# Optimization experiments

Measured on AMD Instinct MI355X. Metric: run time of the kernel, lower is better.

The kernel has to match this reference:

```python
import jax, jax.numpy as jnp
import numpy as np

B, T, C = 2, 2048, 1024
H, HS = 16, 64
FF = 4 * C
EPS = 1e-5


def _layernorm(x, w):
    mu = jnp.mean(x, axis=-1, keepdims=True)
    var = jnp.var(x, axis=-1, keepdims=True)
    return (x - mu) / jnp.sqrt(var + EPS) * w


def setup_inputs() -> dict:
    key = jax.random.key(0)
    ks = jax.random.split(key, 16)
    s_in = 1.0 / np.sqrt(C)
    s_o = 1.0 / np.sqrt(H * HS)
    s_ff = 1.0 / np.sqrt(FF)
    return {
        "x": jax.random.normal(ks[0], (B, T, C), dtype=jnp.float32),
        "ln1_w": jnp.ones((C,), jnp.float32),
        "Wq": jax.random.uniform(ks[1], (H, C, HS), jnp.float32, -s_in, s_in),
        "bq": jax.random.uniform(ks[2], (H, HS), jnp.float32, -s_in, s_in),
        "Wk": jax.random.uniform(ks[3], (H, C, HS), jnp.float32, -s_in, s_in),
        "bk": jax.random.uniform(ks[4], (H, HS), jnp.float32, -s_in, s_in),
        "Wv": jax.random.uniform(ks[5], (H, C, HS), jnp.float32, -s_in, s_in),
        "bv": jax.random.uniform(ks[6], (H, HS), jnp.float32, -s_in, s_in),
        "Wo": jax.random.uniform(ks[7], (H * HS, C), jnp.float32, -s_o, s_o),
        "bo": jax.random.uniform(ks[8], (C,), jnp.float32, -s_o, s_o),
        "ln2_w": jnp.ones((C,), jnp.float32),
        "W1": jax.random.uniform(ks[9], (C, FF), jnp.float32, -s_in, s_in),
        "b1": jax.random.uniform(ks[10], (FF,), jnp.float32, -s_in, s_in),
        "W2": jax.random.uniform(ks[11], (FF, C), jnp.float32, -s_ff, s_ff),
        "b2": jax.random.uniform(ks[12], (C,), jnp.float32, -s_ff, s_ff),
    }


def reference(x, ln1_w, Wq, bq, Wk, bk, Wv, bv, Wo, bo, ln2_w, W1, b1, W2, b2):
    h = _layernorm(x, ln1_w)                                   # [B,T,C]
    q = jnp.einsum("btc,hcd->bhtd", h, Wq) + bq[:, None, :]    # [B,H,T,HS]
    k = jnp.einsum("btc,hcd->bhtd", h, Wk) + bk[:, None, :]
    v = jnp.einsum("btc,hcd->bhtd", h, Wv) + bv[:, None, :]
    scores = jnp.einsum("bhid,bhjd->bhij", q, k) * (HS ** -0.5)
    causal = jnp.tril(jnp.ones((T, T), bool))                  # tril mask
    scores = jnp.where(causal, scores, -jnp.inf)
    # NOTE: original applies softmax over torch dim=1 of [B,T,T] = query axis i
    w = jax.nn.softmax(scores, axis=2)                         # [B,H,i,j]
    att = jnp.einsum("bhij,bhjd->bhid", w, v)                  # [B,H,T,HS]
    att = att.transpose(0, 2, 1, 3).reshape(B, T, H * HS)      # concat heads
    att = att @ Wo + bo                                        # [B,T,C]
    x1 = x + att
    h2 = _layernorm(x1, ln2_w)
    ff = jax.nn.relu(h2 @ W1 + b1) @ W2 + b2
    return x1 + ff
```

## Files before the change

### kernel.cpp

```cpp
#include <hip/hip_runtime.h>
#include <hip/hip_bf16.h>
#include <stddef.h>
#include <stdint.h>


constexpr int Bn = 2, Tn = 2048, Cn = 1024, Hn = 16, HSn = 64, FFn = 4096;
constexpr int Mn = Bn * Tn;
constexpr float EPSf = 1e-5f;
constexpr float S2 = 0.125f * 1.44269504088896340736f;

using short8 = __attribute__((ext_vector_type(8))) short;
using f32x4  = __attribute__((ext_vector_type(4))) float;
using s16x4  = __attribute__((ext_vector_type(4))) short;

#define DEVINL __device__ __forceinline__

DEVINL unsigned short f2bf(float f) {
  unsigned int u = __float_as_uint(f);
  u += 0x7fffu + ((u >> 16) & 1u);
  return (unsigned short)(u >> 16);
}

#define GLDS16(g, l) __builtin_amdgcn_global_load_lds(                        \
    (const __attribute__((address_space(1))) void*)(g),                       \
    (__attribute__((address_space(3))) void*)(l), 16, 0, 0)

__global__ __launch_bounds__(256)
void transpose_cvt(const float* __restrict__ in, unsigned short* __restrict__ out,
                   int R, int S, long zin, long zout) {
  __shared__ float tile[32][33];
  const int c0 = blockIdx.x * 32;
  const int r0 = blockIdx.y * 32;
  in  += (size_t)blockIdx.z * zin;
  out += (size_t)blockIdx.z * zout;
  const int tid = threadIdx.x;
#pragma unroll
  for (int j = 0; j < 4; ++j) {
    const int f = tid + j * 256;
    tile[f >> 5][f & 31] = in[(size_t)(r0 + (f >> 5)) * S + c0 + (f & 31)];
  }
  __syncthreads();
#pragma unroll
  for (int j = 0; j < 4; ++j) {
    const int f = tid + j * 256;
    const int sr = f >> 5, rc = f & 31;
    out[(size_t)(c0 + sr) * R + r0 + rc] = f2bf(tile[rc][sr]);
  }
}

__global__ __launch_bounds__(256)
void ln_bf16(const float* __restrict__ x, const float* __restrict__ w,
             unsigned short* __restrict__ out) {
  const int row = blockIdx.x, tid = threadIdx.x;
  const float4 v = ((const float4*)(x + (size_t)row * Cn))[tid];
  float s  = v.x + v.y + v.z + v.w;
  float ss = v.x*v.x + v.y*v.y + v.z*v.z + v.w*v.w;
#pragma unroll
  for (int o = 32; o > 0; o >>= 1) { s += __shfl_xor(s, o); ss += __shfl_xor(ss, o); }
  __shared__ float red[8];
  if ((tid & 63) == 0) { red[tid >> 6] = s; red[(tid >> 6) + 4] = ss; }
  __syncthreads();
  s  = red[0] + red[1] + red[2] + red[3];
  ss = red[4] + red[5] + red[6] + red[7];
  const float mu   = s * (1.0f / Cn);
  const float rstd = rsqrtf(ss * (1.0f / Cn) - mu * mu + EPSf);
  const float4 wv = ((const float4*)w)[tid];
  s16x4 o;
  o[0] = (short)f2bf((v.x - mu) * rstd * wv.x);
  o[1] = (short)f2bf((v.y - mu) * rstd * wv.y);
  o[2] = (short)f2bf((v.z - mu) * rstd * wv.z);
  o[3] = (short)f2bf((v.w - mu) * rstd * wv.w);
  ((s16x4*)(out + (size_t)row * Cn))[tid] = o;
}

template <int EPI, int OMODE>
__global__ __launch_bounds__(256)
void gemm_bf16(const unsigned short* __restrict__ A,
               const unsigned short* __restrict__ Bt,
               const float* __restrict__ bias, const float* __restrict__ res,
               void* __restrict__ outp, int M, int N, int K) {
  __shared__ unsigned short As[128][64];
  __shared__ unsigned short Bs[128][64];
  const int tid = threadIdx.x;
  const int w = tid >> 6, l = tid & 63;
  const int wm = w >> 1, wn = w & 1;
  const int m0 = blockIdx.y * 128, n0 = blockIdx.x * 128;
  f32x4 acc[4][4];
#pragma unroll
  for (int i = 0; i < 4; ++i)
#pragma unroll
    for (int j = 0; j < 4; ++j) acc[i][j] = (f32x4){0.f, 0.f, 0.f, 0.f};

  for (int k0 = 0; k0 < K; k0 += 64) {
    __syncthreads();
#pragma unroll
    for (int j = 0; j < 4; ++j) {
      const int chunk = (w * 4 + j) * 64 + l;
      const int row = chunk >> 3, slot = chunk & 7;
      GLDS16(A + (size_t)(m0 + row) * K + k0 + ((slot ^ (row & 7)) << 3),
             &As[0][0] + (size_t)(w * 4 + j) * 512);
    }
#pragma unroll
    for (int j = 0; j < 4; ++j) {
      const int chunk = (w * 4 + j) * 64 + l;
      const int row = chunk >> 3, slot = chunk & 7;
      GLDS16(Bt + (size_t)(n0 + row) * K + k0 + ((slot ^ (row & 7)) << 3),
             &Bs[0][0] + (size_t)(w * 4 + j) * 512);
    }
    __syncthreads();
#pragma unroll
    for (int kk = 0; kk < 2; ++kk) {
      short8 a[4], b[4];
#pragma unroll
      for (int i = 0; i < 4; ++i) {
        const int ar = wm * 64 + i * 16 + (l & 15);
        a[i] = *(const short8*)&As[ar][(((l >> 4) + kk * 4) ^ (ar & 7)) << 3];
        const int br = wn * 64 + i * 16 + (l & 15);
        b[i] = *(const short8*)&Bs[br][(((l >> 4) + kk * 4) ^ (br & 7)) << 3];
      }
#pragma unroll
      for (int mi = 0; mi < 4; ++mi)
#pragma unroll
        for (int ni = 0; ni < 4; ++ni)
          acc[mi][ni] = __builtin_amdgcn_mfma_f32_16x16x32_bf16(
              a[mi], b[ni], acc[mi][ni], 0, 0, 0);
    }
  }
  if (OMODE == 2) {
    unsigned short* vT = (unsigned short*)outp;
#pragma unroll
    for (int mi = 0; mi < 4; ++mi)
#pragma unroll
      for (int ni = 0; ni < 4; ++ni) {
        const int n = n0 + wn * 64 + ni * 16 + (l & 15);
        const int mbase = m0 + wm * 64 + mi * 16 + ((l >> 4) << 2);
        const int bb = mbase >> 11, t = mbase & 2047;
        const float bv = bias[n];
        unsigned short* dst = vT + ((size_t)(bb * 1024 + n)) * Tn + t;
        unsigned int p0 = (unsigned)f2bf(acc[mi][ni][0] + bv) |
                          ((unsigned)f2bf(acc[mi][ni][1] + bv) << 16);
        unsigned int p1 = (unsigned)f2bf(acc[mi][ni][2] + bv) |
                          ((unsigned)f2bf(acc[mi][ni][3] + bv) << 16);
        *(unsigned int*)dst       = p0;
        *(unsigned int*)(dst + 2) = p1;
      }
  } else {
#pragma unroll
    for (int mi = 0; mi < 4; ++mi)
#pragma unroll
      for (int ni = 0; ni < 4; ++ni) {
        const int n = n0 + wn * 64 + ni * 16 + (l & 15);
        const float bv = bias[n];
#pragma unroll
        for (int r = 0; r < 4; ++r) {
          const int m = m0 + wm * 64 + mi * 16 + ((l >> 4) << 2) + r;
          float v = acc[mi][ni][r] + bv;
          if (EPI == 1) v = fmaxf(v, 0.f);
          if (EPI == 2) v += res[(size_t)m * N + n];
          if (OMODE == 1) ((unsigned short*)outp)[(size_t)m * N + n] = f2bf(v);
          else            ((float*)outp)[(size_t)m * N + n] = v;
        }
      }
  }
}

DEVINL void stage64s(unsigned short* lds, const unsigned short* g, int grs,
                     int w, int l) {
#pragma unroll
  for (int j = 0; j < 2; ++j) {
    const int chunk = (w * 2 + j) * 64 + l;
    const int row = chunk >> 3, slot = chunk & 7;
    GLDS16(g + (size_t)row * grs + ((slot ^ (row & 7)) << 3),
           lds + (size_t)(w * 2 + j) * 512);
  }
}

__global__ __launch_bounds__(256)
void colstats_mfma(const unsigned short* __restrict__ qk,
                   float* __restrict__ m2buf, float* __restrict__ rlbuf) {
  __shared__ unsigned short Ks[64][64];
  __shared__ unsigned short Qs[64][64];
  __shared__ float redm[4][4][16], redl[4][4][16];
  const int j0 = blockIdx.x * 64;
  const int bh = blockIdx.y, b = bh >> 4, h = bh & 15;
  const int tid = threadIdx.x, w = tid >> 6, l = tid & 63;
  const unsigned short* kbase = qk + ((size_t)(b * Tn + j0)) * 2048 + 1024 + h * 64;
  const unsigned short* qbase = qk + ((size_t)(b * Tn)) * 2048 + h * 64;
  stage64s(&Ks[0][0], kbase, 2048, w, l);
  float m2[4], ls[4];
#pragma unroll
  for (int ni = 0; ni < 4; ++ni) { m2[ni] = -1e30f; ls[ni] = 0.f; }

  for (int i0 = j0; i0 < Tn; i0 += 64) {
    __syncthreads();
    stage64s(&Qs[0][0], qbase + (size_t)i0 * 2048, 2048, w, l);
    __syncthreads();
    f32x4 s[4];
#pragma unroll
    for (int ni = 0; ni < 4; ++ni) s[ni] = (f32x4){0.f, 0.f, 0.f, 0.f};
#pragma unroll
    for (int kk = 0; kk < 2; ++kk) {
      const int ar = w * 16 + (l & 15);
      const short8 af = *(const short8*)&Qs[ar][(((l >> 4) + kk * 4) ^ (ar & 7)) << 3];
#pragma unroll
      for (int ni = 0; ni < 4; ++ni) {
        const int br = ni * 16 + (l & 15);
        const short8 bfr = *(const short8*)&Ks[br][(((l >> 4) + kk * 4) ^ (br & 7)) << 3];
        s[ni] = __builtin_amdgcn_mfma_f32_16x16x32_bf16(af, bfr, s[ni], 0, 0, 0);
      }
    }
    const bool diag = (i0 == j0);
    const int ib = w * 16 + ((l >> 4) << 2);
#pragma unroll
    for (int ni = 0; ni < 4; ++ni) {
      const int jl = ni * 16 + (l & 15);
      float v0 = s[ni][0] * S2, v1 = s[ni][1] * S2, v2 = s[ni][2] * S2, v3 = s[ni][3] * S2;
      if (!diag) {
        const float tmax = fmaxf(fmaxf(v0, v1), fmaxf(v2, v3));
        const float mn = fmaxf(m2[ni], tmax);
        ls[ni] = ls[ni] * exp2f(m2[ni] - mn) +
                 exp2f(v0 - mn) + exp2f(v1 - mn) + exp2f(v2 - mn) + exp2f(v3 - mn);
        m2[ni] = mn;
      } else {
        const bool g0 = (ib + 0 >= jl), g1 = (ib + 1 >= jl), g2 = (ib + 2 >= jl), g3 = (ib + 3 >= jl);
        const float t0 = g0 ? v0 : -1e30f, t1 = g1 ? v1 : -1e30f;
        const float t2 = g2 ? v2 : -1e30f, t3 = g3 ? v3 : -1e30f;
        const float tmax = fmaxf(fmaxf(t0, t1), fmaxf(t2, t3));
        const float mn = fmaxf(m2[ni], tmax);
        const float e0 = g0 ? exp2f(v0 - mn) : 0.f;
        const float e1 = g1 ? exp2f(v1 - mn) : 0.f;
        const float e2 = g2 ? exp2f(v2 - mn) : 0.f;
        const float e3 = g3 ? exp2f(v3 - mn) : 0.f;
        ls[ni] = ls[ni] * exp2f(m2[ni] - mn) + e0 + e1 + e2 + e3;
        m2[ni] = mn;
      }
    }
  }
#pragma unroll
  for (int ni = 0; ni < 4; ++ni) {
#pragma unroll
    for (int off = 16; off < 64; off <<= 1) {
      const float mo = __shfl_xor(m2[ni], off);
      const float lo = __shfl_xor(ls[ni], off);
      const float mn = fmaxf(m2[ni], mo);
      ls[ni] = ls[ni] * exp2f(m2[ni] - mn) + lo * exp2f(mo - mn);
      m2[ni] = mn;
    }
  }
  if (l < 16) {
#pragma unroll
    for (int ni = 0; ni < 4; ++ni) { redm[w][ni][l] = m2[ni]; redl[w][ni][l] = ls[ni]; }
  }
  __syncthreads();
  if (tid < 64) {
    const int ni = tid >> 4, jl = tid & 15;
    float m = redm[0][ni][jl], sl = redl[0][ni][jl];
#pragma unroll
    for (int wv = 1; wv < 4; ++wv) {
      const float mo = redm[wv][ni][jl], lo = redl[wv][ni][jl];
      const float mn = fmaxf(m, mo);
      sl = sl * exp2f(m - mn) + lo * exp2f(mo - mn);
      m = mn;
    }
    m2buf[(size_t)bh * Tn + j0 + ni * 16 + jl] = m;
    rlbuf[(size_t)bh * Tn + j0 + ni * 16 + jl] = 1.0f / sl;
  }
}

__global__ __launch_bounds__(256)
void pv_mfma(const unsigned short* __restrict__ qk,
             const unsigned short* __restrict__ vT,
             const float* __restrict__ m2buf, const float* __restrict__ rlbuf,
             unsigned short* __restrict__ att) {
  __shared__ unsigned short Qs[64][64];
  __shared__ unsigned short Ks[64][64];
  __shared__ unsigned short Vs[64][64];
  __shared__ unsigned short Ps[64][64];
  __shared__ float m2s[64], rls[64];
  const int i0 = blockIdx.x * 64;
  const int bh = blockIdx.y, b = bh >> 4, h = bh & 15;
  const int tid = threadIdx.x, w = tid >> 6, l = tid & 63;
  const unsigned short* qbase = qk + ((size_t)(b * Tn + i0)) * 2048 + h * 64;
  const unsigned short* kbase = qk + ((size_t)(b * Tn)) * 2048 + 1024 + h * 64;
  const unsigned short* vbase = vT + ((size_t)(b * 1024 + h * 64)) * Tn;
  stage64s(&Qs[0][0], qbase, 2048, w, l);
  f32x4 oacc[4];
#pragma unroll
  for (int ni = 0; ni < 4; ++ni) oacc[ni] = (f32x4){0.f, 0.f, 0.f, 0.f};

  for (int j0 = 0; j0 <= i0; j0 += 64) {
    __syncthreads();
    stage64s(&Ks[0][0], kbase + (size_t)j0 * 2048, 2048, w, l);
#pragma unroll
    for (int j = 0; j < 2; ++j) {
      const int chunk = (w * 2 + j) * 64 + l;
      const int row = chunk >> 3, slot = chunk & 7;
      GLDS16(vbase + (size_t)row * Tn + j0 + ((slot ^ (row & 7)) << 3),
             &Vs[0][0] + (size_t)(w * 2 + j) * 512);
    }
    if (tid < 64) {
      m2s[tid] = m2buf[(size_t)bh * Tn + j0 + tid];
      rls[tid] = rlbuf[(size_t)bh * Tn + j0 + tid];
    }
    __syncthreads();
    f32x4 s[4];
#pragma unroll
    for (int ni = 0; ni < 4; ++ni) s[ni] = (f32x4){0.f, 0.f, 0.f, 0.f};
#pragma unroll
    for (int kk = 0; kk < 2; ++kk) {
      const int ar = w * 16 + (l & 15);
      const short8 af = *(const short8*)&Qs[ar][(((l >> 4) + kk * 4) ^ (ar & 7)) << 3];
#pragma unroll
      for (int ni = 0; ni < 4; ++ni) {
        const int br = ni * 16 + (l & 15);
        const short8 bfr = *(const short8*)&Ks[br][(((l >> 4) + kk * 4) ^ (br & 7)) << 3];
        s[ni] = __builtin_amdgcn_mfma_f32_16x16x32_bf16(af, bfr, s[ni], 0, 0, 0);
      }
    }
    const bool diag = (j0 == i0);
    const int ib = w * 16 + ((l >> 4) << 2);
    unsigned short* Pf = &Ps[0][0];
#pragma unroll
    for (int ni = 0; ni < 4; ++ni) {
      const int jl = ni * 16 + (l & 15);
      const float mj = m2s[jl], rj = rls[jl];
#pragma unroll
      for (int r = 0; r < 4; ++r) {
        float p = exp2f(s[ni][r] * S2 - mj) * rj;
        if (diag && (ib + r < jl)) p = 0.f;
        const int il = ib + r;
        Pf[il * 64 + (((jl >> 3) ^ (il & 7)) << 3) + (jl & 7)] = f2bf(p);
      }
    }
#pragma unroll
    for (int kk = 0; kk < 2; ++kk) {
      const int ar = w * 16 + (l & 15);
      const short8 pf = *(const short8*)&Ps[ar][(((l >> 4) + kk * 4) ^ (ar & 7)) << 3];
#pragma unroll
      for (int ni = 0; ni < 4; ++ni) {
        const int br = ni * 16 + (l & 15);
        const short8 vf = *(const short8*)&Vs[br][(((l >> 4) + kk * 4) ^ (br & 7)) << 3];
        oacc[ni] = __builtin_amdgcn_mfma_f32_16x16x32_bf16(pf, vf, oacc[ni], 0, 0, 0);
      }
    }
  }
#pragma unroll
  for (int ni = 0; ni < 4; ++ni) {
    const int col = h * 64 + ni * 16 + (l & 15);
#pragma unroll
    for (int r = 0; r < 4; ++r) {
      const int m = b * Tn + i0 + w * 16 + ((l >> 4) << 2) + r;
      att[(size_t)m * 1024 + col] = f2bf(oacc[ni][r]);
    }
  }
}

extern "C" void kernel_launch(void* const* d_in, const int* in_sizes, int n_in,
                              void* d_out, int out_size, void* d_ws, size_t ws_size,
                              hipStream_t stream) {
  const float* x    = (const float*)d_in[0];
  const float* ln1w = (const float*)d_in[1];
  const float* Wq   = (const float*)d_in[2];
  const float* bq   = (const float*)d_in[3];
  const float* Wk   = (const float*)d_in[4];
  const float* bk   = (const float*)d_in[5];
  const float* Wv   = (const float*)d_in[6];
  const float* bv   = (const float*)d_in[7];
  const float* Wo   = (const float*)d_in[8];
  const float* bo   = (const float*)d_in[9];
  const float* ln2w = (const float*)d_in[10];
  const float* W1   = (const float*)d_in[11];
  const float* b1   = (const float*)d_in[12];
  const float* W2   = (const float*)d_in[13];
  const float* b2   = (const float*)d_in[14];

  uint8_t* wsb = (uint8_t*)d_ws;
  unsigned short* h     = (unsigned short*)(wsb);
  unsigned short* qkb   = (unsigned short*)(wsb + (8ull  << 20));
  unsigned short* vT    = (unsigned short*)(wsb + (24ull << 20));
  unsigned short* attb  = (unsigned short*)(wsb + (32ull << 20));
  float*          x1    = (float*)         (wsb + (40ull << 20));
  unsigned short* ffmid = qkb;
  unsigned short* Wqkt  = (unsigned short*)(wsb + (56ull << 20));
  unsigned short* Wvt   = (unsigned short*)(wsb + (60ull << 20));
  unsigned short* Wot   = (unsigned short*)(wsb + (62ull << 20));
  unsigned short* W1t   = (unsigned short*)(wsb + (64ull << 20));
  unsigned short* W2t   = (unsigned short*)(wsb + (72ull << 20));
  float*          biasqk= (float*)         (wsb + (80ull << 20));
  float*          m2buf = (float*)         (wsb + (81ull << 20));
  float*          rlbuf = (float*)         (wsb + (81ull << 20) + (256ull << 10));

  transpose_cvt<<<dim3(2, 32, 16), 256, 0, stream>>>(Wq, Wqkt,               1024, 64, 65536, 65536);
  transpose_cvt<<<dim3(2, 32, 16), 256, 0, stream>>>(Wk, Wqkt + 1024 * 1024, 1024, 64, 65536, 65536);
  transpose_cvt<<<dim3(2, 32, 16), 256, 0, stream>>>(Wv, Wvt,                1024, 64, 65536, 65536);
  transpose_cvt<<<dim3(32, 32, 1), 256, 0, stream>>>(Wo, Wot,  1024, 1024, 0, 0);
  transpose_cvt<<<dim3(128, 32, 1), 256, 0, stream>>>(W1, W1t, 1024, 4096, 0, 0);
  transpose_cvt<<<dim3(32, 128, 1), 256, 0, stream>>>(W2, W2t, 4096, 1024, 0, 0);
  hipMemcpyAsync(biasqk,        bq, 1024 * sizeof(float), hipMemcpyDeviceToDevice, stream);
  hipMemcpyAsync(biasqk + 1024, bk, 1024 * sizeof(float), hipMemcpyDeviceToDevice, stream);

  ln_bf16<<<Mn, 256, 0, stream>>>(x, ln1w, h);
  gemm_bf16<0, 1><<<dim3(16, 32), 256, 0, stream>>>(h, Wqkt, biasqk, nullptr, qkb, Mn, 2048, Cn);
  gemm_bf16<0, 2><<<dim3(8, 32), 256, 0, stream>>>(h, Wvt, bv, nullptr, vT, Mn, 1024, Cn);
  colstats_mfma<<<dim3(Tn / 64, Bn * Hn), 256, 0, stream>>>(qkb, m2buf, rlbuf);
  pv_mfma<<<dim3(Tn / 64, Bn * Hn), 256, 0, stream>>>(qkb, vT, m2buf, rlbuf, attb);
  gemm_bf16<2, 0><<<dim3(8, 32), 256, 0, stream>>>(attb, Wot, bo, x, x1, Mn, 1024, Cn);
  ln_bf16<<<Mn, 256, 0, stream>>>(x1, ln2w, h);
  gemm_bf16<1, 1><<<dim3(32, 32), 256, 0, stream>>>(h, W1t, b1, nullptr, ffmid, Mn, FFn, Cn);
  gemm_bf16<2, 0><<<dim3(8, 32), 256, 0, stream>>>(ffmid, W2t, b2, x1, (float*)d_out, Mn, Cn, FFn);
}
```

Baseline: 479.6 us.

## Double-buffer GEMM LDS tiles, remap workgroups per XCD, fuse QKV projection

The bf16 GEMM now keeps two LDS stages, so the async global-to-LDS loads for the next K tile are issued while MFMAs run on the current one. This replaces the load/sync/compute/sync sequence that left loads and math serialized. Workgroup IDs are remapped so consecutive tiles land on the same XCD, aiming for better L2 reuse of shared A and B panels. The separate QK and V projection GEMMs are merged into one N=3072 GEMM with a split epilogue that writes row-major QK and transposed V. The cost is doubled LDS per block (64 KB), which may reduce occupancy.

```diff
diff --git a/kernel.cpp b/kernel.cpp
--- a/kernel.cpp
+++ b/kernel.cpp
@@ -79,44 +79,49 @@
                const unsigned short* __restrict__ Bt,
                const float* __restrict__ bias, const float* __restrict__ res,
                void* __restrict__ outp, int M, int N, int K) {
-  __shared__ unsigned short As[128][64];
-  __shared__ unsigned short Bs[128][64];
+  __shared__ unsigned short As[2][128][64];
+  __shared__ unsigned short Bs[2][128][64];
   const int tid = threadIdx.x;
   const int w = tid >> 6, l = tid & 63;
   const int wm = w >> 1, wn = w & 1;
-  const int m0 = blockIdx.y * 128, n0 = blockIdx.x * 128;
+  const int gx = gridDim.x, nwg = gx * gridDim.y;
+  int wg = blockIdx.y * gx + blockIdx.x;
+  {
+    const int q = nwg >> 3, r = nwg & 7;
+    const int xcd = wg & 7, off = wg >> 3;
+    wg = (xcd < r ? xcd * (q + 1) : r * (q + 1) + (xcd - r) * q) + off;
+  }
+  const int m0 = (wg / gx) * 128, n0 = (wg % gx) * 128;
+
   f32x4 acc[4][4];
 #pragma unroll
   for (int i = 0; i < 4; ++i)
 #pragma unroll
     for (int j = 0; j < 4; ++j) acc[i][j] = (f32x4){0.f, 0.f, 0.f, 0.f};
 
-  for (int k0 = 0; k0 < K; k0 += 64) {
-    __syncthreads();
+  const unsigned short* Abase = A + (size_t)m0 * K;
+  const unsigned short* Bbase = Bt + (size_t)n0 * K;
+
+  auto STAGE = [&](unsigned short* as, unsigned short* bs, int k0) {
 #pragma unroll
     for (int j = 0; j < 4; ++j) {
       const int chunk = (w * 4 + j) * 64 + l;
       const int row = chunk >> 3, slot = chunk & 7;
-      GLDS16(A + (size_t)(m0 + row) * K + k0 + ((slot ^ (row & 7)) << 3),
-             &As[0][0] + (size_t)(w * 4 + j) * 512);
-    }
-#pragma unroll
-    for (int j = 0; j < 4; ++j) {
-      const int chunk = (w * 4 + j) * 64 + l;
-      const int row = chunk >> 3, slot = chunk & 7;
-      GLDS16(Bt + (size_t)(n0 + row) * K + k0 + ((slot ^ (row & 7)) << 3),
-             &Bs[0][0] + (size_t)(w * 4 + j) * 512);
-    }
-    __syncthreads();
+      const size_t go = (size_t)row * K + k0 + ((slot ^ (row & 7)) << 3);
+      GLDS16(Abase + go, as + (size_t)(w * 4 + j) * 512);
+      GLDS16(Bbase + go, bs + (size_t)(w * 4 + j) * 512);
+    }
+  };
+  auto COMPUTE = [&](const unsigned short (*as)[64], const unsigned short (*bs)[64]) {
 #pragma unroll
     for (int kk = 0; kk < 2; ++kk) {
       short8 a[4], b[4];
 #pragma unroll
       for (int i = 0; i < 4; ++i) {
         const int ar = wm * 64 + i * 16 + (l & 15);
-        a[i] = *(const short8*)&As[ar][(((l >> 4) + kk * 4) ^ (ar & 7)) << 3];
+        a[i] = *(const short8*)&as[ar][(((l >> 4) + kk * 4) ^ (ar & 7)) << 3];
         const int br = wn * 64 + i * 16 + (l & 15);
-        b[i] = *(const short8*)&Bs[br][(((l >> 4) + kk * 4) ^ (br & 7)) << 3];
+        b[i] = *(const short8*)&bs[br][(((l >> 4) + kk * 4) ^ (br & 7)) << 3];
       }
 #pragma unroll
       for (int mi = 0; mi < 4; ++mi)
@@ -125,25 +130,59 @@
           acc[mi][ni] = __builtin_amdgcn_mfma_f32_16x16x32_bf16(
               a[mi], b[ni], acc[mi][ni], 0, 0, 0);
     }
-  }
-  if (OMODE == 2) {
-    unsigned short* vT = (unsigned short*)outp;
-#pragma unroll
-    for (int mi = 0; mi < 4; ++mi)
-#pragma unroll
-      for (int ni = 0; ni < 4; ++ni) {
-        const int n = n0 + wn * 64 + ni * 16 + (l & 15);
-        const int mbase = m0 + wm * 64 + mi * 16 + ((l >> 4) << 2);
-        const int bb = mbase >> 11, t = mbase & 2047;
-        const float bv = bias[n];
-        unsigned short* dst = vT + ((size_t)(bb * 1024 + n)) * Tn + t;
-        unsigned int p0 = (unsigned)f2bf(acc[mi][ni][0] + bv) |
-                          ((unsigned)f2bf(acc[mi][ni][1] + bv) << 16);
-        unsigned int p1 = (unsigned)f2bf(acc[mi][ni][2] + bv) |
-                          ((unsigned)f2bf(acc[mi][ni][3] + bv) << 16);
-        *(unsigned int*)dst       = p0;
-        *(unsigned int*)(dst + 2) = p1;
-      }
+  };
+
+  const int nt = K >> 6;
+  STAGE(&As[0][0][0], &Bs[0][0][0], 0);
+  __syncthreads();
+  for (int t = 0; t + 2 < nt; t += 2) {
+    STAGE(&As[1][0][0], &Bs[1][0][0], (t + 1) << 6);
+    COMPUTE(As[0], Bs[0]);
+    __syncthreads();
+    STAGE(&As[0][0][0], &Bs[0][0][0], (t + 2) << 6);
+    COMPUTE(As[1], Bs[1]);
+    __syncthreads();
+  }
+  STAGE(&As[1][0][0], &Bs[1][0][0], (nt - 1) << 6);
+  COMPUTE(As[0], Bs[0]);
+  __syncthreads();
+  COMPUTE(As[1], Bs[1]);
+
+  if (OMODE == 3) {
+    if (n0 < 2048) {
+      unsigned short* qk = (unsigned short*)outp;
+#pragma unroll
+      for (int mi = 0; mi < 4; ++mi)
+#pragma unroll
+        for (int ni = 0; ni < 4; ++ni) {
+          const int n = n0 + wn * 64 + ni * 16 + (l & 15);
+          const float bv = bias[n];
+#pragma unroll
+          for (int r = 0; r < 4; ++r) {
+            const int m = m0 + wm * 64 + mi * 16 + ((l >> 4) << 2) + r;
+            qk[(size_t)m * 2048 + n] = f2bf(acc[mi][ni][r] + bv);
+          }
+        }
+    } else {
+      unsigned short* vT = (unsigned short*)outp + (size_t)Mn * 2048;
+#pragma unroll
+      for (int mi = 0; mi < 4; ++mi)
+#pragma unroll
+        for (int ni = 0; ni < 4; ++ni) {
+          const int n = n0 + wn * 64 + ni * 16 + (l & 15);
+          const int nl = n - 2048;
+          const int mbase = m0 + wm * 64 + mi * 16 + ((l >> 4) << 2);
+          const int bb = mbase >> 11, t = mbase & 2047;
+          const float bv = bias[n];
+          unsigned short* dst = vT + ((size_t)(bb * 1024 + nl)) * Tn + t;
+          unsigned int p0 = (unsigned)f2bf(acc[mi][ni][0] + bv) |
+                            ((unsigned)f2bf(acc[mi][ni][1] + bv) << 16);
+          unsigned int p1 = (unsigned)f2bf(acc[mi][ni][2] + bv) |
+                            ((unsigned)f2bf(acc[mi][ni][3] + bv) << 16);
+          *(unsigned int*)dst       = p0;
+          *(unsigned int*)(dst + 2) = p1;
+        }
+    }
   } else {
 #pragma unroll
     for (int mi = 0; mi < 4; ++mi)
@@ -381,27 +420,26 @@
   unsigned short* attb  = (unsigned short*)(wsb + (32ull << 20));
   float*          x1    = (float*)         (wsb + (40ull << 20));
   unsigned short* ffmid = qkb;
-  unsigned short* Wqkt  = (unsigned short*)(wsb + (56ull << 20));
-  unsigned short* Wvt   = (unsigned short*)(wsb + (60ull << 20));
+  unsigned short* Wqkvt = (unsigned short*)(wsb + (56ull << 20));
   unsigned short* Wot   = (unsigned short*)(wsb + (62ull << 20));
   unsigned short* W1t   = (unsigned short*)(wsb + (64ull << 20));
   unsigned short* W2t   = (unsigned short*)(wsb + (72ull << 20));
-  float*          biasqk= (float*)         (wsb + (80ull << 20));
+  float*          biasqkv=(float*)         (wsb + (80ull << 20));
   float*          m2buf = (float*)         (wsb + (81ull << 20));
   float*          rlbuf = (float*)         (wsb + (81ull << 20) + (256ull << 10));
 
-  transpose_cvt<<<dim3(2, 32, 16), 256, 0, stream>>>(Wq, Wqkt,               1024, 64, 65536, 65536);
-  transpose_cvt<<<dim3(2, 32, 16), 256, 0, stream>>>(Wk, Wqkt + 1024 * 1024, 1024, 64, 65536, 65536);
-  transpose_cvt<<<dim3(2, 32, 16), 256, 0, stream>>>(Wv, Wvt,                1024, 64, 65536, 65536);
+  transpose_cvt<<<dim3(2, 32, 16), 256, 0, stream>>>(Wq, Wqkvt,                  1024, 64, 65536, 65536);
+  transpose_cvt<<<dim3(2, 32, 16), 256, 0, stream>>>(Wk, Wqkvt + 1024 * 1024,    1024, 64, 65536, 65536);
+  transpose_cvt<<<dim3(2, 32, 16), 256, 0, stream>>>(Wv, Wqkvt + 2 * 1024 * 1024, 1024, 64, 65536, 65536);
   transpose_cvt<<<dim3(32, 32, 1), 256, 0, stream>>>(Wo, Wot,  1024, 1024, 0, 0);
   transpose_cvt<<<dim3(128, 32, 1), 256, 0, stream>>>(W1, W1t, 1024, 4096, 0, 0);
   transpose_cvt<<<dim3(32, 128, 1), 256, 0, stream>>>(W2, W2t, 4096, 1024, 0, 0);
-  hipMemcpyAsync(biasqk,        bq, 1024 * sizeof(float), hipMemcpyDeviceToDevice, stream);
-  hipMemcpyAsync(biasqk + 1024, bk, 1024 * sizeof(float), hipMemcpyDeviceToDevice, stream);
+  hipMemcpyAsync(biasqkv,        bq, 1024 * sizeof(float), hipMemcpyDeviceToDevice, stream);
+  hipMemcpyAsync(biasqkv + 1024, bk, 1024 * sizeof(float), hipMemcpyDeviceToDevice, stream);
+  hipMemcpyAsync(biasqkv + 2048, bv, 1024 * sizeof(float), hipMemcpyDeviceToDevice, stream);
 
   ln_bf16<<<Mn, 256, 0, stream>>>(x, ln1w, h);
-  gemm_bf16<0, 1><<<dim3(16, 32), 256, 0, stream>>>(h, Wqkt, biasqk, nullptr, qkb, Mn, 2048, Cn);
-  gemm_bf16<0, 2><<<dim3(8, 32), 256, 0, stream>>>(h, Wvt, bv, nullptr, vT, Mn, 1024, Cn);
+  gemm_bf16<0, 3><<<dim3(24, 32), 256, 0, stream>>>(h, Wqkvt, biasqkv, nullptr, qkb, Mn, 3072, Cn);
   colstats_mfma<<<dim3(Tn / 64, Bn * Hn), 256, 0, stream>>>(qkb, m2buf, rlbuf);
   pv_mfma<<<dim3(Tn / 64, Bn * Hn), 256, 0, stream>>>(qkb, vT, m2buf, rlbuf, attb);
   gemm_bf16<2, 0><<<dim3(8, 32), 256, 0, stream>>>(attb, Wot, bo, x, x1, Mn, 1024, Cn);
```

Result: no change. 482.7 us (+0.6%).
